# Optimization experiments

Hardware: AMD Instinct MI355X
Metric: run time of the kernel (lower is better)

## Reference

```python
import jax, jax.numpy as jnp
import numpy as np

N_NODES = 50000
N_EDGES = 1200000
D_FEAT = 64
HIDDEN = 32


def setup_inputs() -> dict:
    key = jax.random.key(0)
    ks = jax.random.split(key, 9)
    x = jax.random.normal(ks[0], (N_NODES, D_FEAT), dtype=jnp.float32)
    edge_index = jax.random.randint(ks[1], (2, N_EDGES), 0, N_NODES, dtype=jnp.int64)
    u = jax.random.normal(ks[2], (N_NODES,), dtype=jnp.float32)
    d_in = 2 * D_FEAT
    # MLP: Linear(d_in,H) -> relu -> Linear(H,H) -> relu -> Linear(H,1)
    W1 = jax.random.normal(ks[3], (d_in, HIDDEN), dtype=jnp.float32) / np.sqrt(d_in)
    b1 = jnp.zeros((HIDDEN,), dtype=jnp.float32)
    W2 = jax.random.normal(ks[4], (HIDDEN, HIDDEN), dtype=jnp.float32) / np.sqrt(HIDDEN)
    b2 = jnp.zeros((HIDDEN,), dtype=jnp.float32)
    W3 = jax.random.normal(ks[5], (HIDDEN, 1), dtype=jnp.float32) / np.sqrt(HIDDEN)
    b3 = jnp.zeros((1,), dtype=jnp.float32)
    return {"x": x, "edge_index": edge_index, "u": u,
            "W1": W1, "b1": b1, "W2": W2, "b2": b2, "W3": W3, "b3": b3}


def reference(x, edge_index, u, W1, b1, W2, b2, W3, b3):
    row, col = edge_index[0], edge_index[1]
    # gather + concat: [E, 2*D]
    x_edge = jnp.concatenate([x[row], x[col]], axis=-1)
    # per-edge MLP -> scalar weight per edge
    h = jax.nn.relu(x_edge @ W1 + b1)
    h = jax.nn.relu(h @ W2 + b2)
    edge_weight = (h @ W3 + b3)[:, 0]  # [E]
    # spmm: f[i] = sum_{e: row[e]==i} w_e * u[col[e]]
    f = jax.ops.segment_sum(edge_weight * u[col], row, num_segments=x.shape[0])
    return f
```

## Files before the change

kernel.cpp:

```cpp
#include <hip/hip_runtime.h>

#define N_NODES 50000
#define N_EDGES 1200000
#define N_TILES (N_NODES / 16)
#define N_REP   16
#define REP_STRIDE 50064
#define W1T_STRIDE 72

typedef __attribute__((ext_vector_type(8))) short short8;
typedef __attribute__((ext_vector_type(4))) float floatx4;

__device__ __forceinline__ unsigned short f32_to_bf16(float f) {
    unsigned int u = __float_as_uint(f);
    unsigned int r = u + 0x7FFFu + ((u >> 16) & 1u);
    return (unsigned short)(r >> 16);
}
__device__ __forceinline__ float bf16_to_f32(unsigned short s) {
    return __uint_as_float(((unsigned int)s) << 16);
}
__device__ __forceinline__ unsigned int pack_bf16x2(float lo, float hi) {
    return (unsigned int)f32_to_bf16(lo) | ((unsigned int)f32_to_bf16(hi) << 16);
}

__global__ __launch_bounds__(256) void precompute_P_mfma(
    const float* __restrict__ x, const float* __restrict__ W1,
    const float* __restrict__ b1, unsigned short* __restrict__ P)
{
    __shared__ unsigned short W1t[64 * W1T_STRIDE];
    const int tid = threadIdx.x;
    for (int e = tid; e < 128 * 32; e += 256) {
        const int kp = e >> 5, jp = e & 31;
        const int k = kp & 63;
        const int j = (kp < 64) ? jp : jp + 32;
        W1t[j * W1T_STRIDE + k] = f32_to_bf16(W1[e]);
    }
    __syncthreads();

    const int lane = tid & 63;
    const int n = lane & 15;
    const int q = lane >> 4;

    short8 bf[4][2];
    #pragma unroll
    for (int G = 0; G < 4; ++G)
        #pragma unroll
        for (int h = 0; h < 2; ++h)
            bf[G][h] = *(const short8*)&W1t[(n + 16 * G) * W1T_STRIDE + h * 32 + q * 8];

    const float bias0 = b1[n], bias1 = b1[n + 16];

    unsigned int* P32 = (unsigned int*)P;

    const int wid0   = blockIdx.x * 4 + (tid >> 6);
    const int stride = gridDim.x * 4;
    for (int tile = wid0; tile < N_TILES; tile += stride) {
        const int node = tile * 16 + n;
        const float4* xp  = (const float4*)(x + (size_t)node * 64 + q * 8);
        const float4 xa = xp[0], xb = xp[1];
        const float4* xp2 = (const float4*)(x + (size_t)node * 64 + 32 + q * 8);
        const float4 xc = xp2[0], xd = xp2[1];

        short8 a0, a1;
        a0[0] = (short)f32_to_bf16(xa.x); a0[1] = (short)f32_to_bf16(xa.y);
        a0[2] = (short)f32_to_bf16(xa.z); a0[3] = (short)f32_to_bf16(xa.w);
        a0[4] = (short)f32_to_bf16(xb.x); a0[5] = (short)f32_to_bf16(xb.y);
        a0[6] = (short)f32_to_bf16(xb.z); a0[7] = (short)f32_to_bf16(xb.w);
        a1[0] = (short)f32_to_bf16(xc.x); a1[1] = (short)f32_to_bf16(xc.y);
        a1[2] = (short)f32_to_bf16(xc.z); a1[3] = (short)f32_to_bf16(xc.w);
        a1[4] = (short)f32_to_bf16(xd.x); a1[5] = (short)f32_to_bf16(xd.y);
        a1[6] = (short)f32_to_bf16(xd.z); a1[7] = (short)f32_to_bf16(xd.w);

        floatx4 acc[4];
        #pragma unroll
        for (int G = 0; G < 4; ++G) {
            const float bi = (G == 0) ? bias0 : (G == 1) ? bias1 : 0.0f;
            acc[G] = (floatx4){bi, bi, bi, bi};
            acc[G] = __builtin_amdgcn_mfma_f32_16x16x32_bf16(a0, bf[G][0], acc[G], 0, 0, 0);
            acc[G] = __builtin_amdgcn_mfma_f32_16x16x32_bf16(a1, bf[G][1], acc[G], 0, 0, 0);
        }
        #pragma unroll
        for (int r = 0; r < 4; ++r) {
            const int nr = tile * 16 + q * 4 + r;
            P32[(size_t)nr * 32 + n]      = pack_bf16x2(acc[0][r], acc[1][r]);
            P32[(size_t)nr * 32 + 16 + n] = pack_bf16x2(acc[2][r], acc[3][r]);
        }
    }
}

__global__ __launch_bounds__(256) void edge_mlp_mfma(
    const int* __restrict__ row, const int* __restrict__ col,
    const float* __restrict__ u,
    const float* __restrict__ W2, const float* __restrict__ b2,
    const float* __restrict__ W3, const float* __restrict__ b3,
    const unsigned short* __restrict__ P, float* __restrict__ rep)
{
    const int lane = threadIdx.x & 63;
    const int n = lane & 15;
    const int q = lane >> 4;

    short8 bf0, bf1;
    #pragma unroll
    for (int i = 0; i < 8; ++i) {
        const int F = q * 4 + (i >> 1) + 16 * (i & 1);
        bf0[i] = (short)f32_to_bf16(W2[F * 32 + n]);
        bf1[i] = (short)f32_to_bf16(W2[F * 32 + n + 16]);
    }
    const float w3n0 = W3[n], w3n1 = W3[n + 16];
    const float b2n0 = b2[n], b2n1 = b2[n + 16];
    const float bias3 = b3[0];

    const int wave   = (blockIdx.x * 256 + (int)threadIdx.x) >> 6;
    const int nwaves = gridDim.x * 4;
    const int nchunks = N_EDGES / 32;
    float* myrep = rep + (size_t)(wave & (N_REP - 1)) * REP_STRIDE;

    for (int ch = wave; ch < nchunks; ch += nwaves) {
        const int base0 = ch * 32;

        int rI[2], cI[2];
        #pragma unroll
        for (int t = 0; t < 2; ++t) {
            const int e = base0 + t * 16 + n;
            rI[t] = row[e];
            cI[t] = col[e];
        }
        int r2 = 0; float u2 = 0.0f;
        if (n < 8) {
            const int e2 = base0 + 16 * (n >> 2) + 4 * q + (n & 3);
            r2 = row[e2];
            u2 = u[col[e2]];
        }
        short8 v1[2], v2[2];
        #pragma unroll
        for (int t = 0; t < 2; ++t) {
            v1[t] = *(const short8*)(P + (size_t)rI[t] * 64 + q * 8);
            v2[t] = *(const short8*)(P + (size_t)cI[t] * 64 + 32 + q * 8);
        }

        float tr[2][4];
        #pragma unroll
        for (int t = 0; t < 2; ++t) {
            short8 a;
            #pragma unroll
            for (int i = 0; i < 8; ++i) {
                const float f1 = bf16_to_f32((unsigned short)v1[t][i]);
                const float f2 = bf16_to_f32((unsigned short)v2[t][i]);
                a[i] = (short)f32_to_bf16(fmaxf(f1 + f2, 0.0f));
            }
            floatx4 d0 = {b2n0, b2n0, b2n0, b2n0};
            floatx4 d1 = {b2n1, b2n1, b2n1, b2n1};
            d0 = __builtin_amdgcn_mfma_f32_16x16x32_bf16(a, bf0, d0, 0, 0, 0);
            d1 = __builtin_amdgcn_mfma_f32_16x16x32_bf16(a, bf1, d1, 0, 0, 0);
            #pragma unroll
            for (int r = 0; r < 4; ++r)
                tr[t][r] = fmaxf(d0[r], 0.0f) * w3n0 + fmaxf(d1[r], 0.0f) * w3n1;
        }

        #pragma unroll
        for (int mask = 1; mask < 16; mask <<= 1) {
            #pragma unroll
            for (int t = 0; t < 2; ++t)
                #pragma unroll
                for (int r = 0; r < 4; ++r)
                    tr[t][r] += __shfl_xor(tr[t][r], mask, 64);
        }

        if (n < 8) {
            const float va0 = (n & 4) ? tr[1][0] : tr[0][0];
            const float va1 = (n & 4) ? tr[1][1] : tr[0][1];
            const float va2 = (n & 4) ? tr[1][2] : tr[0][2];
            const float va3 = (n & 4) ? tr[1][3] : tr[0][3];
            const float vb0 = (n & 2) ? va2 : va0;
            const float vb1 = (n & 2) ? va3 : va1;
            const float v   = (n & 1) ? vb1 : vb0;
            atomicAdd(myrep + r2, (v + bias3) * u2);
        }
    }
}

__global__ __launch_bounds__(256) void reduce_out(
    const float* __restrict__ rep, float* __restrict__ out)
{
    const int i = blockIdx.x * 256 + (int)threadIdx.x;
    if (i < N_NODES) {
        float s = 0.0f;
        #pragma unroll
        for (int r = 0; r < N_REP; ++r)
            s += rep[(size_t)r * REP_STRIDE + i];
        out[i] = s;
    }
}

extern "C" void kernel_launch(void* const* d_in, const int* in_sizes, int n_in,
                              void* d_out, int out_size, void* d_ws, size_t ws_size,
                              hipStream_t stream)
{
    const float* x    = (const float*)d_in[0];
    const int*   eidx = (const int*)  d_in[1];
    const float* u    = (const float*)d_in[2];
    const float* W1   = (const float*)d_in[3];
    const float* b1   = (const float*)d_in[4];
    const float* W2   = (const float*)d_in[5];
    const float* b2   = (const float*)d_in[6];
    const float* W3   = (const float*)d_in[7];
    const float* b3   = (const float*)d_in[8];

    const int* row = eidx;
    const int* col = eidx + N_EDGES;

    unsigned short* P = (unsigned short*)d_ws;
    float* rep = (float*)((char*)d_ws + (size_t)N_NODES * 128);
    float* out = (float*)d_out;

    hipMemsetAsync(rep, 0, (size_t)N_REP * REP_STRIDE * sizeof(float), stream);

    precompute_P_mfma<<<512, 256, 0, stream>>>(x, W1, b1, P);

    edge_mlp_mfma<<<1024, 256, 0, stream>>>(
        row, col, u, W2, b2, W3, b3, P, rep);

    reduce_out<<<(N_NODES + 255) / 256, 256, 0, stream>>>(rep, out);
}
```

Before: 153.1 us.

## Drop replicated scatter buffers, atomically accumulate into output, one-shot edge waves

Removes the 16-way replicated atomic accumulation buffers, the memset and the final reduction kernel. Output zeroing now happens inside the precompute kernel and edges atomically add straight into out. The edge kernel becomes non-persistent: each wave handles two 32-edge chunks with all index and P loads issued up front, and it gets a launch bound of 4 blocks per SIMD. This saves two launches and the replica traffic, but every atomic now lands on a single array, so contention on hot rows can rise.

```diff
diff --git a/kernel.cpp b/kernel.cpp
--- a/kernel.cpp
+++ b/kernel.cpp
@@ -3,16 +3,17 @@
 #define N_NODES 50000
 #define N_EDGES 1200000
 #define N_TILES (N_NODES / 16)
-#define N_REP   16
-#define REP_STRIDE 50064
 #define W1T_STRIDE 72
+#define NCHUNKS (N_EDGES / 32)
+#define EDGE_WAVES ((NCHUNKS + 1) / 2)
+#define EDGE_BLOCKS ((EDGE_WAVES + 3) / 4)
 
 typedef __attribute__((ext_vector_type(8))) short short8;
 typedef __attribute__((ext_vector_type(4))) float floatx4;
 
 __device__ __forceinline__ unsigned short f32_to_bf16(float f) {
-    unsigned int u = __float_as_uint(f);
-    unsigned int r = u + 0x7FFFu + ((u >> 16) & 1u);
+    unsigned int v = __float_as_uint(f);
+    unsigned int r = v + 0x7FFFu + ((v >> 16) & 1u);
     return (unsigned short)(r >> 16);
 }
 __device__ __forceinline__ float bf16_to_f32(unsigned short s) {
@@ -24,15 +25,20 @@
 
 __global__ __launch_bounds__(256) void precompute_P_mfma(
     const float* __restrict__ x, const float* __restrict__ W1,
-    const float* __restrict__ b1, unsigned short* __restrict__ P)
+    const float* __restrict__ b1, unsigned short* __restrict__ P,
+    float* __restrict__ out)
 {
+    const int tid  = threadIdx.x;
+    const int gtid = blockIdx.x * 256 + tid;
+
+    for (int i = gtid; i < N_NODES; i += gridDim.x * 256)
+        out[i] = 0.0f;
+
     __shared__ unsigned short W1t[64 * W1T_STRIDE];
-    const int tid = threadIdx.x;
     for (int e = tid; e < 128 * 32; e += 256) {
         const int kp = e >> 5, jp = e & 31;
-        const int k = kp & 63;
-        const int j = (kp < 64) ? jp : jp + 32;
-        W1t[j * W1T_STRIDE + k] = f32_to_bf16(W1[e]);
+        W1t[((kp < 64) ? jp : jp + 32) * W1T_STRIDE + (kp & 63)] =
+            f32_to_bf16(W1[e]);
     }
     __syncthreads();
 
@@ -40,17 +46,16 @@
     const int n = lane & 15;
     const int q = lane >> 4;
 
-    short8 bf[4][2];
+    short8 bw[4][2];
     #pragma unroll
     for (int G = 0; G < 4; ++G)
         #pragma unroll
         for (int h = 0; h < 2; ++h)
-            bf[G][h] = *(const short8*)&W1t[(n + 16 * G) * W1T_STRIDE + h * 32 + q * 8];
-
+            bw[G][h] = *(const short8*)
+                &W1t[(n + 16 * G) * W1T_STRIDE + h * 32 + q * 8];
     const float bias0 = b1[n], bias1 = b1[n + 16];
 
     unsigned int* P32 = (unsigned int*)P;
-
     const int wid0   = blockIdx.x * 4 + (tid >> 6);
     const int stride = gridDim.x * 4;
     for (int tile = wid0; tile < N_TILES; tile += stride) {
@@ -75,8 +80,8 @@
         for (int G = 0; G < 4; ++G) {
             const float bi = (G == 0) ? bias0 : (G == 1) ? bias1 : 0.0f;
             acc[G] = (floatx4){bi, bi, bi, bi};
-            acc[G] = __builtin_amdgcn_mfma_f32_16x16x32_bf16(a0, bf[G][0], acc[G], 0, 0, 0);
-            acc[G] = __builtin_amdgcn_mfma_f32_16x16x32_bf16(a1, bf[G][1], acc[G], 0, 0, 0);
+            acc[G] = __builtin_amdgcn_mfma_f32_16x16x32_bf16(a0, bw[G][0], acc[G], 0, 0, 0);
+            acc[G] = __builtin_amdgcn_mfma_f32_16x16x32_bf16(a1, bw[G][1], acc[G], 0, 0, 0);
         }
         #pragma unroll
         for (int r = 0; r < 4; ++r) {
@@ -87,16 +92,38 @@
     }
 }
 
-__global__ __launch_bounds__(256) void edge_mlp_mfma(
+__global__ __launch_bounds__(256, 4) void edge_mlp_mfma(
     const int* __restrict__ row, const int* __restrict__ col,
     const float* __restrict__ u,
     const float* __restrict__ W2, const float* __restrict__ b2,
     const float* __restrict__ W3, const float* __restrict__ b3,
-    const unsigned short* __restrict__ P, float* __restrict__ rep)
+    const unsigned short* __restrict__ P, float* __restrict__ out)
 {
-    const int lane = threadIdx.x & 63;
+    const int tid  = threadIdx.x;
+    const int lane = tid & 63;
     const int n = lane & 15;
     const int q = lane >> 4;
+
+    const int wave = (blockIdx.x * 256 + tid) >> 6;
+    const int c = wave * 2;
+    if (c >= NCHUNKS) return;
+
+    int rI[4], cI[4];
+    #pragma unroll
+    for (int t = 0; t < 4; ++t) {
+        const int e = c * 32 + t * 16 + n;
+        rI[t] = row[e];
+        cI[t] = col[e];
+    }
+    int r2[2]; float u2[2];
+    if (n < 8) {
+        #pragma unroll
+        for (int p = 0; p < 2; ++p) {
+            const int e2 = (c + p) * 32 + 16 * (n >> 2) + 4 * q + (n & 3);
+            r2[p] = row[e2];
+            u2[p] = u[col[e2]];
+        }
+    }
 
     short8 bf0, bf1;
     #pragma unroll
@@ -109,85 +136,53 @@
     const float b2n0 = b2[n], b2n1 = b2[n + 16];
     const float bias3 = b3[0];
 
-    const int wave   = (blockIdx.x * 256 + (int)threadIdx.x) >> 6;
-    const int nwaves = gridDim.x * 4;
-    const int nchunks = N_EDGES / 32;
-    float* myrep = rep + (size_t)(wave & (N_REP - 1)) * REP_STRIDE;
-
-    for (int ch = wave; ch < nchunks; ch += nwaves) {
-        const int base0 = ch * 32;
-
-        int rI[2], cI[2];
-        #pragma unroll
-        for (int t = 0; t < 2; ++t) {
-            const int e = base0 + t * 16 + n;
-            rI[t] = row[e];
-            cI[t] = col[e];
-        }
-        int r2 = 0; float u2 = 0.0f;
-        if (n < 8) {
-            const int e2 = base0 + 16 * (n >> 2) + 4 * q + (n & 3);
-            r2 = row[e2];
-            u2 = u[col[e2]];
-        }
-        short8 v1[2], v2[2];
-        #pragma unroll
-        for (int t = 0; t < 2; ++t) {
-            v1[t] = *(const short8*)(P + (size_t)rI[t] * 64 + q * 8);
-            v2[t] = *(const short8*)(P + (size_t)cI[t] * 64 + 32 + q * 8);
-        }
-
-        float tr[2][4];
-        #pragma unroll
-        for (int t = 0; t < 2; ++t) {
-            short8 a;
-            #pragma unroll
-            for (int i = 0; i < 8; ++i) {
-                const float f1 = bf16_to_f32((unsigned short)v1[t][i]);
-                const float f2 = bf16_to_f32((unsigned short)v2[t][i]);
-                a[i] = (short)f32_to_bf16(fmaxf(f1 + f2, 0.0f));
-            }
-            floatx4 d0 = {b2n0, b2n0, b2n0, b2n0};
-            floatx4 d1 = {b2n1, b2n1, b2n1, b2n1};
-            d0 = __builtin_amdgcn_mfma_f32_16x16x32_bf16(a, bf0, d0, 0, 0, 0);
-            d1 = __builtin_amdgcn_mfma_f32_16x16x32_bf16(a, bf1, d1, 0, 0, 0);
+    short8 v1[4], v2[4];
+    #pragma unroll
+    for (int t = 0; t < 4; ++t) {
+        v1[t] = *(const short8*)(P + (size_t)rI[t] * 64 + q * 8);
+        v2[t] = *(const short8*)(P + (size_t)cI[t] * 64 + 32 + q * 8);
+    }
+
+    float tr[4][4];
+    #pragma unroll
+    for (int t = 0; t < 4; ++t) {
+        short8 a;
+        #pragma unroll
+        for (int i = 0; i < 8; ++i) {
+            const float f1 = bf16_to_f32((unsigned short)v1[t][i]);
+            const float f2 = bf16_to_f32((unsigned short)v2[t][i]);
+            a[i] = (short)f32_to_bf16(fmaxf(f1 + f2, 0.0f));
+        }
+        floatx4 d0 = {b2n0, b2n0, b2n0, b2n0};
+        floatx4 d1 = {b2n1, b2n1, b2n1, b2n1};
+        d0 = __builtin_amdgcn_mfma_f32_16x16x32_bf16(a, bf0, d0, 0, 0, 0);
+        d1 = __builtin_amdgcn_mfma_f32_16x16x32_bf16(a, bf1, d1, 0, 0, 0);
+        #pragma unroll
+        for (int r = 0; r < 4; ++r)
+            tr[t][r] = fmaxf(d0[r], 0.0f) * w3n0 + fmaxf(d1[r], 0.0f) * w3n1;
+    }
+
+    #pragma unroll
+    for (int mask = 1; mask < 16; mask <<= 1)
+        #pragma unroll
+        for (int t = 0; t < 4; ++t)
             #pragma unroll
             for (int r = 0; r < 4; ++r)
-                tr[t][r] = fmaxf(d0[r], 0.0f) * w3n0 + fmaxf(d1[r], 0.0f) * w3n1;
-        }
-
-        #pragma unroll
-        for (int mask = 1; mask < 16; mask <<= 1) {
-            #pragma unroll
-            for (int t = 0; t < 2; ++t)
-                #pragma unroll
-                for (int r = 0; r < 4; ++r)
-                    tr[t][r] += __shfl_xor(tr[t][r], mask, 64);
-        }
-
-        if (n < 8) {
-            const float va0 = (n & 4) ? tr[1][0] : tr[0][0];
-            const float va1 = (n & 4) ? tr[1][1] : tr[0][1];
-            const float va2 = (n & 4) ? tr[1][2] : tr[0][2];
-            const float va3 = (n & 4) ? tr[1][3] : tr[0][3];
+                tr[t][r] += __shfl_xor(tr[t][r], mask, 64);
+
+    if (n < 8) {
+        #pragma unroll
+        for (int p = 0; p < 2; ++p) {
+            const int tb = 2 * p;
+            const float va0 = (n & 4) ? tr[tb + 1][0] : tr[tb][0];
+            const float va1 = (n & 4) ? tr[tb + 1][1] : tr[tb][1];
+            const float va2 = (n & 4) ? tr[tb + 1][2] : tr[tb][2];
+            const float va3 = (n & 4) ? tr[tb + 1][3] : tr[tb][3];
             const float vb0 = (n & 2) ? va2 : va0;
             const float vb1 = (n & 2) ? va3 : va1;
             const float v   = (n & 1) ? vb1 : vb0;
-            atomicAdd(myrep + r2, (v + bias3) * u2);
-        }
-    }
-}
-
-__global__ __launch_bounds__(256) void reduce_out(
-    const float* __restrict__ rep, float* __restrict__ out)
-{
-    const int i = blockIdx.x * 256 + (int)threadIdx.x;
-    if (i < N_NODES) {
-        float s = 0.0f;
-        #pragma unroll
-        for (int r = 0; r < N_REP; ++r)
-            s += rep[(size_t)r * REP_STRIDE + i];
-        out[i] = s;
+            atomicAdd(out + r2[p], (v + bias3) * u2[p]);
+        }
     }
 }
 
@@ -209,15 +204,10 @@
     const int* col = eidx + N_EDGES;
 
     unsigned short* P = (unsigned short*)d_ws;
-    float* rep = (float*)((char*)d_ws + (size_t)N_NODES * 128);
     float* out = (float*)d_out;
 
-    hipMemsetAsync(rep, 0, (size_t)N_REP * REP_STRIDE * sizeof(float), stream);
-
-    precompute_P_mfma<<<512, 256, 0, stream>>>(x, W1, b1, P);
-
-    edge_mlp_mfma<<<1024, 256, 0, stream>>>(
-        row, col, u, W2, b2, W3, b3, P, rep);
-
-    reduce_out<<<(N_NODES + 255) / 256, 256, 0, stream>>>(rep, out);
-}
+    precompute_P_mfma<<<512, 256, 0, stream>>>(x, W1, b1, P, out);
+
+    edge_mlp_mfma<<<EDGE_BLOCKS, 256, 0, stream>>>(
+        row, col, u, W2, b2, W3, b3, P, out);
+}
```

New measurement: 166.4 us. 1.09x slower.
